# Kernel optimization log

Measured on AMD Instinct MI355X. Metric: run time of the kernel, lower is better.

## Reference

```python
import jax, jax.numpy as jnp
import numpy as np

N_HEAD = 16
QK_NOPE = 128
QK_ROPE = 64
QK_HEAD = QK_NOPE + QK_ROPE  # 192
V_HEAD = 128
SCALE = 1.0 / np.sqrt(QK_HEAD)


def setup_inputs() -> dict:
    key = jax.random.key(0)
    ks = jax.random.split(key, 8)
    B, T, C = 2, 2048, 2048
    s = lambda fan: 1.0 / np.sqrt(fan)
    return {
        "x": jax.random.normal(ks[0], (B, T, C), jnp.float32),
        "freqs_cis": jax.random.uniform(ks[1], (T, QK_ROPE // 2, 2), jnp.float32),
        "w_q": jax.random.normal(ks[2], (C, N_HEAD * QK_HEAD), jnp.float32) * s(C),
        "w_kv_down": jax.random.normal(ks[3], (C, 256), jnp.float32) * s(C),
        "w_k_up": jax.random.normal(ks[4], (256, N_HEAD * QK_HEAD), jnp.float32) * s(256),
        "w_v_up": jax.random.normal(ks[5], (256, N_HEAD * V_HEAD), jnp.float32) * s(256),
        "w_o": jax.random.normal(ks[6], (N_HEAD * V_HEAD, C), jnp.float32) * s(N_HEAD * V_HEAD),
        "start_pos": 0,
    }


def _rotate_half(x):
    x1, x2 = x[..., : x.shape[-1] // 2], x[..., x.shape[-1] // 2 :]
    return jnp.concatenate([-x2, x1], axis=-1)


def reference(x, freqs_cis, w_q, w_kv_down, w_k_up, w_v_up, w_o, start_pos):
    B, T, C = x.shape
    # low-rank MLA projections
    q = (x @ w_q).reshape(B, T, N_HEAD, QK_HEAD)
    kv = x @ w_kv_down                                  # (B,T,r)
    k = (kv @ w_k_up).reshape(B, T, N_HEAD, QK_HEAD)
    v = (kv @ w_v_up).reshape(B, T, N_HEAD, V_HEAD)

    # inline RoPE on decoupled rope dims
    q_nope, q_rope = q[..., :QK_NOPE], q[..., QK_NOPE:]
    k_nope, k_rope = k[..., :QK_NOPE], k[..., QK_NOPE:]
    freqs = freqs_cis[start_pos : start_pos + T]         # (T, 32, 2)
    cos = freqs[..., 0][None, :, None, :]                # (1,T,1,32)
    sin = freqs[..., 1][None, :, None, :]
    rep = QK_ROPE // cos.shape[-1]
    cos = jnp.tile(cos, (1, 1, 1, rep))                  # (1,T,1,64)
    sin = jnp.tile(sin, (1, 1, 1, rep))
    q_rope = q_rope * cos + _rotate_half(q_rope) * sin
    k_rope = k_rope * cos + _rotate_half(k_rope) * sin
    q = jnp.concatenate([q_nope, q_rope], axis=-1)
    k = jnp.concatenate([k_nope, k_rope], axis=-1)

    # causal SDPA with mismatched QK vs V head dims
    scores = jnp.einsum("bqhd,bkhd->bhqk", q, k) * SCALE
    causal = jnp.tril(jnp.ones((T, T), dtype=bool))
    scores = jnp.where(causal[None, None], scores, -jnp.inf)
    probs = jax.nn.softmax(scores, axis=-1)
    out = jnp.einsum("bhqk,bkhd->bqhd", probs, v)        # (B,T,H,V_HEAD)
    out = out.reshape(B, T, N_HEAD * V_HEAD)
    return out @ w_o
```

## Files before the change

### kernel.cpp

```cpp
#include <hip/hip_runtime.h>
#include <stdint.h>

typedef unsigned short u16;
typedef float f32x4 __attribute__((ext_vector_type(4)));
typedef __bf16 bf16x8 __attribute__((ext_vector_type(8)));

static __device__ __forceinline__ u16 f2bf(float f) {
  union { float f; unsigned u; } v; v.f = f;
  unsigned r = v.u + 0x7fffu + ((v.u >> 16) & 1u);
  return (u16)(r >> 16);
}
static __device__ __forceinline__ float bf2f(u16 h) {
  union { unsigned u; float f; } v; v.u = ((unsigned)h) << 16;
  return v.f;
}

#define GLD_LDS16(gp, lp) __builtin_amdgcn_global_load_lds( \
    (__attribute__((address_space(1))) void*)(gp),          \
    (__attribute__((address_space(3))) void*)(lp), 16, 0, 0)

#define MFMA16(a, b, c) __builtin_amdgcn_mfma_f32_16x16x32_bf16((a), (b), (c), 0, 0, 0)

__global__ void conv_bf16_kernel(const float* __restrict__ in, u16* __restrict__ out, long n) {
  long stride = (long)gridDim.x * blockDim.x * 4;
  for (long i = ((long)blockIdx.x * blockDim.x + threadIdx.x) * 4; i < n; i += stride) {
    float4 v = *(const float4*)(in + i);
    union { u16 s[4]; uint2 u; } pk;
    pk.s[0] = f2bf(v.x); pk.s[1] = f2bf(v.y); pk.s[2] = f2bf(v.z); pk.s[3] = f2bf(v.w);
    *(uint2*)(out + i) = pk.u;
  }
}

__global__ void transpose_conv_kernel(const float* __restrict__ W, u16* __restrict__ WT,
                                      int K, int N) {
  __shared__ float tile[32][33];
  const int n0 = blockIdx.x * 32, k0 = blockIdx.y * 32;
  const int tx = threadIdx.x, ty = threadIdx.y;
#pragma unroll
  for (int i = 0; i < 32; i += 8) tile[ty + i][tx] = W[(long)(k0 + ty + i) * N + n0 + tx];
  __syncthreads();
#pragma unroll
  for (int i = 0; i < 32; i += 8)
    WT[(long)(n0 + ty + i) * K + k0 + tx] = f2bf(tile[tx][ty + i]);
}

template <bool OUT_F32>
__global__ __launch_bounds__(256, 2)
void gemm_bt_kernel(const u16* __restrict__ A, const u16* __restrict__ BT,
                    void* __restrict__ Cv, int N, int K, long sA, long sB, long sC) {
  const int bz = blockIdx.z;
  A += (long)bz * sA;
  BT += (long)bz * sB;
  const int m0 = blockIdx.y << 7, n0 = blockIdx.x << 7;
  __shared__ alignas(16) u16 lA[128 * 64];
  __shared__ alignas(16) u16 lB[128 * 64];
  const int tid = threadIdx.x;
  const int w = tid >> 6, l = tid & 63;
  const int wr = w >> 1, wc = w & 1;
  const int lrow = l & 15, lg = l >> 4;
  const int srow = l >> 3, scol = (l & 7) << 3;
  f32x4 acc[4][4] = {};
  for (int kt = 0; kt < K; kt += 64) {
    __syncthreads();
#pragma unroll
    for (int i = 0; i < 4; i++) {
      const int chunk = (w << 2) + i;
      const int row = (chunk << 3) + srow;
      GLD_LDS16(A + (long)(m0 + row) * K + kt + scol, &lA[chunk << 9]);
      GLD_LDS16(BT + (long)(n0 + row) * K + kt + scol, &lB[chunk << 9]);
    }
    __syncthreads();
#pragma unroll
    for (int kk = 0; kk < 2; kk++) {
      bf16x8 af[4], bb[4];
#pragma unroll
      for (int i = 0; i < 4; i++) {
        af[i] = *(const bf16x8*)&lA[((wr << 6) + (i << 4) + lrow) * 64 + (kk << 5) + (lg << 3)];
        bb[i] = *(const bf16x8*)&lB[((wc << 6) + (i << 4) + lrow) * 64 + (kk << 5) + (lg << 3)];
      }
#pragma unroll
      for (int mi = 0; mi < 4; mi++)
#pragma unroll
        for (int ni = 0; ni < 4; ni++)
          acc[mi][ni] = MFMA16(af[mi], bb[ni], acc[mi][ni]);
    }
  }
#pragma unroll
  for (int mi = 0; mi < 4; mi++) {
    const int r0 = m0 + (wr << 6) + (mi << 4) + (lg << 2);
#pragma unroll
    for (int ni = 0; ni < 4; ni++) {
      const int c0 = n0 + (wc << 6) + (ni << 4) + lrow;
#pragma unroll
      for (int r = 0; r < 4; r++) {
        const float val = acc[mi][ni][r];
        if constexpr (OUT_F32)
          ((float*)Cv + (long)bz * sC)[(long)(r0 + r) * N + c0] = val;
        else
          ((u16*)Cv + (long)bz * sC)[(long)(r0 + r) * N + c0] = f2bf(val);
      }
    }
  }
}

__device__ __forceinline__ void epilogue_rope_store(
    u16* __restrict__ C, const int N, const f32x4 (*acc)[4],
    const int m0, const int wr, const int wc, const int cbase_wave,
    const int lrow, const int lg, const bool ropewin,
    const float* __restrict__ freqs, const int sp) {
#pragma unroll
  for (int mi = 0; mi < 4; mi++) {
    const int r0 = m0 + (wr << 6) + (mi << 4) + (lg << 2);
#pragma unroll
    for (int r = 0; r < 4; r++) {
      float v0 = acc[mi][0][r], v1 = acc[mi][1][r];
      float v2 = acc[mi][2][r], v3 = acc[mi][3][r];
      if (ropewin) {
        const int t = (r0 + r) & 2047;
        const float2 cs0 = *(const float2*)&freqs[((long)(sp + t) * 32 + lrow) * 2];
        const float2 cs1 = *(const float2*)&freqs[((long)(sp + t) * 32 + 16 + lrow) * 2];
        const float n0v = v0 * cs0.x - v2 * cs0.y;
        const float n1v = v1 * cs1.x - v3 * cs1.y;
        const float n2v = v2 * cs0.x + v0 * cs0.y;
        const float n3v = v3 * cs1.x + v1 * cs1.y;
        v0 = n0v; v1 = n1v; v2 = n2v; v3 = n3v;
      }
      const long ro = (long)(r0 + r) * N + cbase_wave + lrow;
      C[ro] = f2bf(v0);
      C[ro + 16] = f2bf(v1);
      C[ro + 32] = f2bf(v2);
      C[ro + 48] = f2bf(v3);
    }
  }
}

__global__ __launch_bounds__(256, 2)
void gemm_q_kvd_kernel(const u16* __restrict__ A, const u16* __restrict__ wqT,
                       const u16* __restrict__ wkdT, u16* __restrict__ qb,
                       u16* __restrict__ kvb,
                       const float* __restrict__ freqs, const int* __restrict__ sp_ptr) {
  constexpr int K = 2048;
  const int m0 = blockIdx.y << 7;
  const int n0raw = blockIdx.x << 7;
  const bool is_kv = n0raw >= 3072;
  const u16* BT = is_kv ? (wkdT + (long)(n0raw - 3072) * K) : (wqT + (long)n0raw * K);
  u16* C = is_kv ? kvb : qb;
  const int N = is_kv ? 256 : 3072;
  const int c_base = is_kv ? (n0raw - 3072) : n0raw;
  __shared__ alignas(16) u16 lA[128 * 64];
  __shared__ alignas(16) u16 lB[128 * 64];
  const int tid = threadIdx.x;
  const int w = tid >> 6, l = tid & 63;
  const int wr = w >> 1, wc = w & 1;
  const int lrow = l & 15, lg = l >> 4;
  const int srow = l >> 3, scol = (l & 7) << 3;
  f32x4 acc[4][4] = {};
  for (int kt = 0; kt < K; kt += 64) {
    __syncthreads();
#pragma unroll
    for (int i = 0; i < 4; i++) {
      const int chunk = (w << 2) + i;
      const int row = (chunk << 3) + srow;
      GLD_LDS16(A + (long)(m0 + row) * K + kt + scol, &lA[chunk << 9]);
      GLD_LDS16(BT + (long)row * K + kt + scol, &lB[chunk << 9]);
    }
    __syncthreads();
#pragma unroll
    for (int kk = 0; kk < 2; kk++) {
      bf16x8 af[4], bb[4];
#pragma unroll
      for (int i = 0; i < 4; i++) {
        af[i] = *(const bf16x8*)&lA[((wr << 6) + (i << 4) + lrow) * 64 + (kk << 5) + (lg << 3)];
        bb[i] = *(const bf16x8*)&lB[((wc << 6) + (i << 4) + lrow) * 64 + (kk << 5) + (lg << 3)];
      }
#pragma unroll
      for (int mi = 0; mi < 4; mi++)
#pragma unroll
        for (int ni = 0; ni < 4; ni++)
          acc[mi][ni] = MFMA16(af[mi], bb[ni], acc[mi][ni]);
    }
  }
  const int cbase_wave = c_base + (wc << 6);
  const bool ropewin = (!is_kv) && (cbase_wave % 192 == 128);
  const int sp = sp_ptr[0];
  epilogue_rope_store(C, N, acc, m0, wr, wc, cbase_wave, lrow, lg, ropewin, freqs, sp);
}

__global__ __launch_bounds__(256, 2)
void gemm_kup_vt_kernel(const u16* __restrict__ kvb, const u16* __restrict__ wkuT,
                        const u16* __restrict__ wvuT, u16* __restrict__ kb,
                        u16* __restrict__ vTb,
                        const float* __restrict__ freqs, const int* __restrict__ sp_ptr) {
  constexpr int K = 256;
  const int bid = blockIdx.x;
  const u16 *A, *BT;
  u16* C;
  int N, m0, n0;
  bool is_k;
  if (bid < 768) {
    A = kvb; BT = wkuT; C = kb; N = 3072;
    m0 = (bid / 24) << 7; n0 = (bid % 24) << 7;
    is_k = true;
  } else {
    int r = bid - 768;
    const int bz = r >> 8;
    r &= 255;
    A = wvuT; BT = kvb + (long)bz * 2048 * 256; C = vTb + (long)bz * 2048 * 2048;
    N = 2048;
    m0 = (r >> 4) << 7; n0 = (r & 15) << 7;
    is_k = false;
  }
  __shared__ alignas(16) u16 lA[128 * 64];
  __shared__ alignas(16) u16 lB[128 * 64];
  const int tid = threadIdx.x;
  const int w = tid >> 6, l = tid & 63;
  const int wr = w >> 1, wc = w & 1;
  const int lrow = l & 15, lg = l >> 4;
  const int srow = l >> 3, scol = (l & 7) << 3;
  f32x4 acc[4][4] = {};
  for (int kt = 0; kt < K; kt += 64) {
    __syncthreads();
#pragma unroll
    for (int i = 0; i < 4; i++) {
      const int chunk = (w << 2) + i;
      const int row = (chunk << 3) + srow;
      GLD_LDS16(A + (long)(m0 + row) * K + kt + scol, &lA[chunk << 9]);
      GLD_LDS16(BT + (long)(n0 + row) * K + kt + scol, &lB[chunk << 9]);
    }
    __syncthreads();
#pragma unroll
    for (int kk = 0; kk < 2; kk++) {
      bf16x8 af[4], bb[4];
#pragma unroll
      for (int i = 0; i < 4; i++) {
        af[i] = *(const bf16x8*)&lA[((wr << 6) + (i << 4) + lrow) * 64 + (kk << 5) + (lg << 3)];
        bb[i] = *(const bf16x8*)&lB[((wc << 6) + (i << 4) + lrow) * 64 + (kk << 5) + (lg << 3)];
      }
#pragma unroll
      for (int mi = 0; mi < 4; mi++)
#pragma unroll
        for (int ni = 0; ni < 4; ni++)
          acc[mi][ni] = MFMA16(af[mi], bb[ni], acc[mi][ni]);
    }
  }
  const int cbase_wave = n0 + (wc << 6);
  const bool ropewin = is_k && (cbase_wave % 192 == 128);
  const int sp = sp_ptr[0];
  epilogue_rope_store(C, N, acc, m0, wr, wc, cbase_wave, lrow, lg, ropewin, freqs, sp);
}


__device__ __forceinline__ void attn_tile_step(
    const bf16x8* __restrict__ qf, f32x4* __restrict__ o, float* __restrict__ l_part,
    const int qrb, const int t0,
    const u16* __restrict__ Kl, const u16* __restrict__ Vl,
    u16* __restrict__ pw, const int lrow, const int lg) {
  constexpr float SCALE = 0.07216878364870323f;
  f32x4 s[4];
  __builtin_amdgcn_s_setprio(1);
#pragma unroll
  for (int tb = 0; tb < 4; tb++) {
    f32x4 a = {};
#pragma unroll
    for (int kb = 0; kb < 6; kb++) {
      bf16x8 kf = *(const bf16x8*)&Kl[((tb << 4) + lrow) * 200 + (kb << 5) + (lg << 3)];
      a = MFMA16(qf[kb], kf, a);
    }
    s[tb] = a;
  }
  __builtin_amdgcn_s_setprio(0);
#pragma unroll
  for (int tb = 0; tb < 4; tb++) {
    const int tt = t0 + (tb << 4) + lrow;
#pragma unroll
    for (int r = 0; r < 4; r++) {
      const int qrow = qrb + (lg << 2) + r;
      float p = __expf(s[tb][r] * SCALE);
      p = (tt <= qrow) ? p : 0.f;
      s[tb][r] = p;
      l_part[r] += p;
    }
  }
#pragma unroll
  for (int tb = 0; tb < 4; tb++)
#pragma unroll
    for (int r = 0; r < 4; r++)
      pw[((lg << 2) + r) * 68 + (tb << 4) + lrow] = f2bf(s[tb][r]);
  bf16x8 pf0 = *(const bf16x8*)&pw[lrow * 68 + (lg << 3)];
  bf16x8 pf1 = *(const bf16x8*)&pw[lrow * 68 + 32 + (lg << 3)];
  __builtin_amdgcn_s_setprio(1);
#pragma unroll
  for (int db = 0; db < 8; db++) {
    bf16x8 v0 = *(const bf16x8*)&Vl[((db << 4) + lrow) * 72 + (lg << 3)];
    bf16x8 v1 = *(const bf16x8*)&Vl[((db << 4) + lrow) * 72 + 32 + (lg << 3)];
    o[db] = MFMA16(pf0, v0, o[db]);
    o[db] = MFMA16(pf1, v1, o[db]);
  }
  __builtin_amdgcn_s_setprio(0);
}

__device__ __forceinline__ void attn_tile_step2(
    const bf16x8* __restrict__ qfA, const bf16x8* __restrict__ qfB,
    f32x4* __restrict__ oA, f32x4* __restrict__ oB,
    float* __restrict__ lpA, float* __restrict__ lpB,
    const int qrbA, const int qrbB, const int t0,
    const u16* __restrict__ Kl, const u16* __restrict__ Vl,
    u16* __restrict__ pwA, u16* __restrict__ pwB, const int lrow, const int lg) {
  constexpr float SCALE = 0.07216878364870323f;
  f32x4 sA[4], sB[4];
  __builtin_amdgcn_s_setprio(1);
#pragma unroll
  for (int tb = 0; tb < 4; tb++) {
    f32x4 a = {}, bq = {};
#pragma unroll
    for (int kb = 0; kb < 6; kb++) {
      bf16x8 kf = *(const bf16x8*)&Kl[((tb << 4) + lrow) * 200 + (kb << 5) + (lg << 3)];
      a = MFMA16(qfA[kb], kf, a);
      bq = MFMA16(qfB[kb], kf, bq);
    }
    sA[tb] = a;
    sB[tb] = bq;
  }
  __builtin_amdgcn_s_setprio(0);
#pragma unroll
  for (int tb = 0; tb < 4; tb++) {
    const int tt = t0 + (tb << 4) + lrow;
#pragma unroll
    for (int r = 0; r < 4; r++) {
      const int qrowA = qrbA + (lg << 2) + r;
      float pA = __expf(sA[tb][r] * SCALE);
      pA = (tt <= qrowA) ? pA : 0.f;
      sA[tb][r] = pA;
      lpA[r] += pA;
      const int qrowB = qrbB + (lg << 2) + r;
      float pB = __expf(sB[tb][r] * SCALE);
      pB = (tt <= qrowB) ? pB : 0.f;
      sB[tb][r] = pB;
      lpB[r] += pB;
    }
  }
#pragma unroll
  for (int tb = 0; tb < 4; tb++)
#pragma unroll
    for (int r = 0; r < 4; r++) {
      pwA[((lg << 2) + r) * 68 + (tb << 4) + lrow] = f2bf(sA[tb][r]);
      pwB[((lg << 2) + r) * 68 + (tb << 4) + lrow] = f2bf(sB[tb][r]);
    }
  bf16x8 pfA0 = *(const bf16x8*)&pwA[lrow * 68 + (lg << 3)];
  bf16x8 pfA1 = *(const bf16x8*)&pwA[lrow * 68 + 32 + (lg << 3)];
  bf16x8 pfB0 = *(const bf16x8*)&pwB[lrow * 68 + (lg << 3)];
  bf16x8 pfB1 = *(const bf16x8*)&pwB[lrow * 68 + 32 + (lg << 3)];
  __builtin_amdgcn_s_setprio(1);
#pragma unroll
  for (int db = 0; db < 8; db++) {
    bf16x8 v0 = *(const bf16x8*)&Vl[((db << 4) + lrow) * 72 + (lg << 3)];
    bf16x8 v1 = *(const bf16x8*)&Vl[((db << 4) + lrow) * 72 + 32 + (lg << 3)];
    oA[db] = MFMA16(pfA0, v0, oA[db]);
    oB[db] = MFMA16(pfB0, v0, oB[db]);
    oA[db] = MFMA16(pfA1, v1, oA[db]);
    oB[db] = MFMA16(pfB1, v1, oB[db]);
  }
  __builtin_amdgcn_s_setprio(0);
}

__device__ __forceinline__ void attn_write(
    u16* __restrict__ ob, const f32x4* __restrict__ o, const float* __restrict__ l_part,
    const int lrow, const int lg) {
#pragma unroll
  for (int r = 0; r < 4; r++) {
    float l = l_part[r];
#pragma unroll
    for (int d = 1; d < 16; d <<= 1) l += __shfl_xor(l, d);
    const float inv = 1.f / l;
#pragma unroll
    for (int db = 0; db < 8; db++)
      ob[(long)((lg << 2) + r) * 2048 + (db << 4) + lrow] = f2bf(o[db][r] * inv);
  }
}

__global__ __launch_bounds__(256, 2)
void attn_kernel(const u16* __restrict__ q, const u16* __restrict__ k,
                 const u16* __restrict__ vT, u16* __restrict__ out) {
  const int bid = blockIdx.x;
  const int xcd = bid & 7;
  const int rest = bid >> 3;
  const int pair = rest & 15;
  const int bh = ((rest >> 4) << 3) | xcd;
  const int b = bh >> 4, h = bh & 15;
  const int tid = threadIdx.x, w = tid >> 6, l = tid & 63;
  const int lrow = l & 15, lg = l >> 4;
  const int qtA = pair, qtB = 31 - pair;
  const int qrbA = (qtA << 6) + (w << 4);
  const int qrbB = (qtB << 6) + (w << 4);
  __shared__ alignas(16) u16 Kl[64 * 200];
  __shared__ alignas(16) u16 Vl[128 * 72];
  __shared__ alignas(16) u16 Pl[4][2][16 * 68];

  bf16x8 qfA[6], qfB[6];
  {
    const u16* qbA = q + ((long)b * 2048 + qrbA + lrow) * 3072 + h * 192;
    const u16* qbB = q + ((long)b * 2048 + qrbB + lrow) * 3072 + h * 192;
#pragma unroll
    for (int kb = 0; kb < 6; kb++) {
      qfA[kb] = *(const bf16x8*)&qbA[(kb << 5) + (lg << 3)];
      qfB[kb] = *(const bf16x8*)&qbB[(kb << 5) + (lg << 3)];
    }
  }
  f32x4 oA[8] = {}, oB[8] = {};
  float lA[4] = {}, lB[4] = {};

  const u16* kbh = k + (long)b * 2048 * 3072 + h * 192;
  const u16* vbh = vT + ((long)b * 2048 + h * 128) * 2048;
  const int tEndA = qtA << 6, tEndB = qtB << 6;

  for (int t0 = 0; t0 <= tEndB; t0 += 64) {
    __syncthreads();
#pragma unroll
    for (int i = 0; i < 6; i++) {
      int c = (i << 8) + tid;
      int row = c / 24, col = (c % 24) << 3;
      *(bf16x8*)&Kl[row * 200 + col] = *(const bf16x8*)&kbh[(long)(t0 + row) * 3072 + col];
    }
#pragma unroll
    for (int i = 0; i < 4; i++) {
      int c = (i << 8) + tid;
      int row = c >> 3, col = (c & 7) << 3;
      *(bf16x8*)&Vl[row * 72 + col] = *(const bf16x8*)&vbh[(long)row * 2048 + t0 + col];
    }
    __syncthreads();
    if (t0 <= tEndA)
      attn_tile_step2(qfA, qfB, oA, oB, lA, lB, qrbA, qrbB, t0, Kl, Vl,
                      &Pl[w][0][0], &Pl[w][1][0], lrow, lg);
    else
      attn_tile_step(qfB, oB, lB, qrbB, t0, Kl, Vl, &Pl[w][1][0], lrow, lg);
  }
  attn_write(out + ((long)b * 2048 + qrbA) * 2048 + (h << 7), oA, lA, lrow, lg);
  attn_write(out + ((long)b * 2048 + qrbB) * 2048 + (h << 7), oB, lB, lrow, lg);
}

extern "C" void kernel_launch(void* const* d_in, const int* in_sizes, int n_in,
                              void* d_out, int out_size, void* d_ws, size_t ws_size,
                              hipStream_t stream) {
  const float* x = (const float*)d_in[0];
  const float* fcis = (const float*)d_in[1];
  const float* w_q = (const float*)d_in[2];
  const float* w_kvd = (const float*)d_in[3];
  const float* w_ku = (const float*)d_in[4];
  const float* w_vu = (const float*)d_in[5];
  const float* w_o = (const float*)d_in[6];
  const int* start_pos = (const int*)d_in[7];
  float* out = (float*)d_out;

  char* p = (char*)d_ws;
  auto alloc = [&](long bytes) -> char* {
    char* r = p;
    p += (bytes + 255) & ~255ll;
    return r;
  };
  u16* xb = (u16*)alloc(4096ll * 2048 * 2);
  u16* wqT = (u16*)alloc(3072ll * 2048 * 2);
  u16* wkdT = (u16*)alloc(256ll * 2048 * 2);
  u16* wkuT = (u16*)alloc(3072ll * 256 * 2);
  u16* wvuT = (u16*)alloc(2048ll * 256 * 2);
  u16* woT = (u16*)alloc(2048ll * 2048 * 2);
  u16* qb = (u16*)alloc(4096ll * 3072 * 2);
  u16* kvb = (u16*)alloc(4096ll * 256 * 2);
  u16* kb = (u16*)alloc(4096ll * 3072 * 2);
  u16* aob = (u16*)alloc(4096ll * 2048 * 2);
  u16* vTb = xb;

  conv_bf16_kernel<<<2048, 256, 0, stream>>>(x, xb, 4096ll * 2048);
  dim3 tb(32, 8);
  transpose_conv_kernel<<<dim3(3072 / 32, 2048 / 32), tb, 0, stream>>>(w_q, wqT, 2048, 3072);
  transpose_conv_kernel<<<dim3(256 / 32, 2048 / 32), tb, 0, stream>>>(w_kvd, wkdT, 2048, 256);
  transpose_conv_kernel<<<dim3(3072 / 32, 256 / 32), tb, 0, stream>>>(w_ku, wkuT, 256, 3072);
  transpose_conv_kernel<<<dim3(2048 / 32, 256 / 32), tb, 0, stream>>>(w_vu, wvuT, 256, 2048);
  transpose_conv_kernel<<<dim3(2048 / 32, 2048 / 32), tb, 0, stream>>>(w_o, woT, 2048, 2048);

  gemm_q_kvd_kernel<<<dim3(26, 32), 256, 0, stream>>>(xb, wqT, wkdT, qb, kvb, fcis, start_pos);
  gemm_kup_vt_kernel<<<1280, 256, 0, stream>>>(kvb, wkuT, wvuT, kb, vTb, fcis, start_pos);
  attn_kernel<<<512, 256, 0, stream>>>(qb, kb, vTb, aob);
  gemm_bt_kernel<true><<<dim3(16, 32, 1), 256, 0, stream>>>(aob, woT, out, 2048, 2048, 0, 0, 0);
}
```

Baseline: 288.1 us.

## Fuse prep conversions into one launch and remap GEMM tiles per XCD

Merges the x-to-bf16 conversion and the five weight transpose-conversions into a single prep kernel, which removes five kernel launches. It also remaps the block indices of the three GEMM kernels so that each XCD (blocks taken as bid mod 8) gets a contiguous group of M tiles, aiming to improve reuse in the per-XCD L2 cache. The output GEMM becomes a dedicated non-templated kernel with a 1D grid that uses the same swizzle. The change relies on the 1D grid count matching the tile counts exactly.

```diff
diff --git a/kernel.cpp b/kernel.cpp
--- a/kernel.cpp
+++ b/kernel.cpp
@@ -21,86 +21,41 @@
 
 #define MFMA16(a, b, c) __builtin_amdgcn_mfma_f32_16x16x32_bf16((a), (b), (c), 0, 0, 0)
 
-__global__ void conv_bf16_kernel(const float* __restrict__ in, u16* __restrict__ out, long n) {
-  long stride = (long)gridDim.x * blockDim.x * 4;
-  for (long i = ((long)blockIdx.x * blockDim.x + threadIdx.x) * 4; i < n; i += stride) {
-    float4 v = *(const float4*)(in + i);
-    union { u16 s[4]; uint2 u; } pk;
-    pk.s[0] = f2bf(v.x); pk.s[1] = f2bf(v.y); pk.s[2] = f2bf(v.z); pk.s[3] = f2bf(v.w);
-    *(uint2*)(out + i) = pk.u;
-  }
-}
-
-__global__ void transpose_conv_kernel(const float* __restrict__ W, u16* __restrict__ WT,
-                                      int K, int N) {
+__global__ void prep_kernel(const float* __restrict__ x, u16* __restrict__ xb,
+                            const float* __restrict__ w_q, u16* __restrict__ wqT,
+                            const float* __restrict__ w_kvd, u16* __restrict__ wkdT,
+                            const float* __restrict__ w_ku, u16* __restrict__ wkuT,
+                            const float* __restrict__ w_vu, u16* __restrict__ wvuT,
+                            const float* __restrict__ w_o, u16* __restrict__ woT) {
   __shared__ float tile[32][33];
-  const int n0 = blockIdx.x * 32, k0 = blockIdx.y * 32;
+  const int bid = blockIdx.x;
   const int tx = threadIdx.x, ty = threadIdx.y;
+  if (bid < 2048) {
+    const int tid = ty * 32 + tx;
+    const long n = 4096ll * 2048;
+    const long stride = 2048ll * 256 * 4;
+    for (long i = ((long)bid * 256 + tid) * 4; i < n; i += stride) {
+      float4 v = *(const float4*)(x + i);
+      union { u16 s[4]; uint2 u; } pk;
+      pk.s[0] = f2bf(v.x); pk.s[1] = f2bf(v.y); pk.s[2] = f2bf(v.z); pk.s[3] = f2bf(v.w);
+      *(uint2*)(xb + i) = pk.u;
+    }
+    return;
+  }
+  const float* W; u16* WT; int K, N, bx, by;
+  int r = bid - 2048;
+  if (r < 6144)        { W = w_q;   WT = wqT;  K = 2048; N = 3072; bx = r % 96; by = r / 96; }
+  else if ((r -= 6144) < 512) { W = w_kvd; WT = wkdT; K = 2048; N = 256;  bx = r % 8;  by = r / 8; }
+  else if ((r -= 512) < 768)  { W = w_ku;  WT = wkuT; K = 256;  N = 3072; bx = r % 96; by = r / 96; }
+  else if ((r -= 768) < 512)  { W = w_vu;  WT = wvuT; K = 256;  N = 2048; bx = r % 64; by = r / 64; }
+  else                 { r -= 512; W = w_o; WT = woT; K = 2048; N = 2048; bx = r % 64; by = r / 64; }
+  const int n0 = bx * 32, k0 = by * 32;
 #pragma unroll
   for (int i = 0; i < 32; i += 8) tile[ty + i][tx] = W[(long)(k0 + ty + i) * N + n0 + tx];
   __syncthreads();
 #pragma unroll
   for (int i = 0; i < 32; i += 8)
     WT[(long)(n0 + ty + i) * K + k0 + tx] = f2bf(tile[tx][ty + i]);
-}
-
-template <bool OUT_F32>
-__global__ __launch_bounds__(256, 2)
-void gemm_bt_kernel(const u16* __restrict__ A, const u16* __restrict__ BT,
-                    void* __restrict__ Cv, int N, int K, long sA, long sB, long sC) {
-  const int bz = blockIdx.z;
-  A += (long)bz * sA;
-  BT += (long)bz * sB;
-  const int m0 = blockIdx.y << 7, n0 = blockIdx.x << 7;
-  __shared__ alignas(16) u16 lA[128 * 64];
-  __shared__ alignas(16) u16 lB[128 * 64];
-  const int tid = threadIdx.x;
-  const int w = tid >> 6, l = tid & 63;
-  const int wr = w >> 1, wc = w & 1;
-  const int lrow = l & 15, lg = l >> 4;
-  const int srow = l >> 3, scol = (l & 7) << 3;
-  f32x4 acc[4][4] = {};
-  for (int kt = 0; kt < K; kt += 64) {
-    __syncthreads();
-#pragma unroll
-    for (int i = 0; i < 4; i++) {
-      const int chunk = (w << 2) + i;
-      const int row = (chunk << 3) + srow;
-      GLD_LDS16(A + (long)(m0 + row) * K + kt + scol, &lA[chunk << 9]);
-      GLD_LDS16(BT + (long)(n0 + row) * K + kt + scol, &lB[chunk << 9]);
-    }
-    __syncthreads();
-#pragma unroll
-    for (int kk = 0; kk < 2; kk++) {
-      bf16x8 af[4], bb[4];
-#pragma unroll
-      for (int i = 0; i < 4; i++) {
-        af[i] = *(const bf16x8*)&lA[((wr << 6) + (i << 4) + lrow) * 64 + (kk << 5) + (lg << 3)];
-        bb[i] = *(const bf16x8*)&lB[((wc << 6) + (i << 4) + lrow) * 64 + (kk << 5) + (lg << 3)];
-      }
-#pragma unroll
-      for (int mi = 0; mi < 4; mi++)
-#pragma unroll
-        for (int ni = 0; ni < 4; ni++)
-          acc[mi][ni] = MFMA16(af[mi], bb[ni], acc[mi][ni]);
-    }
-  }
-#pragma unroll
-  for (int mi = 0; mi < 4; mi++) {
-    const int r0 = m0 + (wr << 6) + (mi << 4) + (lg << 2);
-#pragma unroll
-    for (int ni = 0; ni < 4; ni++) {
-      const int c0 = n0 + (wc << 6) + (ni << 4) + lrow;
-#pragma unroll
-      for (int r = 0; r < 4; r++) {
-        const float val = acc[mi][ni][r];
-        if constexpr (OUT_F32)
-          ((float*)Cv + (long)bz * sC)[(long)(r0 + r) * N + c0] = val;
-        else
-          ((u16*)Cv + (long)bz * sC)[(long)(r0 + r) * N + c0] = f2bf(val);
-      }
-    }
-  }
 }
 
 __device__ __forceinline__ void epilogue_rope_store(
@@ -140,8 +95,11 @@
                        u16* __restrict__ kvb,
                        const float* __restrict__ freqs, const int* __restrict__ sp_ptr) {
   constexpr int K = 2048;
-  const int m0 = blockIdx.y << 7;
-  const int n0raw = blockIdx.x << 7;
+  const int bid = blockIdx.x;
+  const int xcd = bid & 7;
+  const int idx = bid >> 3;
+  const int m0 = ((xcd << 2) + (idx & 3)) << 7;
+  const int n0raw = (idx >> 2) << 7;
   const bool is_kv = n0raw >= 3072;
   const u16* BT = is_kv ? (wkdT + (long)(n0raw - 3072) * K) : (wqT + (long)n0raw * K);
   u16* C = is_kv ? kvb : qb;
@@ -198,16 +156,20 @@
   int N, m0, n0;
   bool is_k;
   if (bid < 768) {
+    const int xcd = bid & 7, idx = bid >> 3;
     A = kvb; BT = wkuT; C = kb; N = 3072;
-    m0 = (bid / 24) << 7; n0 = (bid % 24) << 7;
+    m0 = ((xcd << 2) + (idx & 3)) << 7;
+    n0 = (idx >> 2) << 7;
     is_k = true;
   } else {
-    int r = bid - 768;
-    const int bz = r >> 8;
-    r &= 255;
+    const int r = bid - 768;
+    const int xcd = r & 7, idx = r >> 3;
+    const int mt = (xcd << 1) + (idx & 1);
+    const int rest = idx >> 1;
+    const int nt = rest & 15, bz = rest >> 4;
     A = wvuT; BT = kvb + (long)bz * 2048 * 256; C = vTb + (long)bz * 2048 * 2048;
     N = 2048;
-    m0 = (r >> 4) << 7; n0 = (r & 15) << 7;
+    m0 = mt << 7; n0 = nt << 7;
     is_k = false;
   }
   __shared__ alignas(16) u16 lA[128 * 64];
@@ -247,6 +209,60 @@
   const bool ropewin = is_k && (cbase_wave % 192 == 128);
   const int sp = sp_ptr[0];
   epilogue_rope_store(C, N, acc, m0, wr, wc, cbase_wave, lrow, lg, ropewin, freqs, sp);
+}
+
+__global__ __launch_bounds__(256, 2)
+void gemm_out_kernel(const u16* __restrict__ A, const u16* __restrict__ BT,
+                     float* __restrict__ C) {
+  constexpr int K = 2048, N = 2048;
+  const int bid = blockIdx.x;
+  const int xcd = bid & 7, idx = bid >> 3;
+  const int m0 = ((xcd << 2) + (idx & 3)) << 7;
+  const int n0 = (idx >> 2) << 7;
+  __shared__ alignas(16) u16 lA[128 * 64];
+  __shared__ alignas(16) u16 lB[128 * 64];
+  const int tid = threadIdx.x;
+  const int w = tid >> 6, l = tid & 63;
+  const int wr = w >> 1, wc = w & 1;
+  const int lrow = l & 15, lg = l >> 4;
+  const int srow = l >> 3, scol = (l & 7) << 3;
+  f32x4 acc[4][4] = {};
+  for (int kt = 0; kt < K; kt += 64) {
+    __syncthreads();
+#pragma unroll
+    for (int i = 0; i < 4; i++) {
+      const int chunk = (w << 2) + i;
+      const int row = (chunk << 3) + srow;
+      GLD_LDS16(A + (long)(m0 + row) * K + kt + scol, &lA[chunk << 9]);
+      GLD_LDS16(BT + (long)(n0 + row) * K + kt + scol, &lB[chunk << 9]);
+    }
+    __syncthreads();
+#pragma unroll
+    for (int kk = 0; kk < 2; kk++) {
+      bf16x8 af[4], bb[4];
+#pragma unroll
+      for (int i = 0; i < 4; i++) {
+        af[i] = *(const bf16x8*)&lA[((wr << 6) + (i << 4) + lrow) * 64 + (kk << 5) + (lg << 3)];
+        bb[i] = *(const bf16x8*)&lB[((wc << 6) + (i << 4) + lrow) * 64 + (kk << 5) + (lg << 3)];
+      }
+#pragma unroll
+      for (int mi = 0; mi < 4; mi++)
+#pragma unroll
+        for (int ni = 0; ni < 4; ni++)
+          acc[mi][ni] = MFMA16(af[mi], bb[ni], acc[mi][ni]);
+    }
+  }
+#pragma unroll
+  for (int mi = 0; mi < 4; mi++) {
+    const int r0 = m0 + (wr << 6) + (mi << 4) + (lg << 2);
+#pragma unroll
+    for (int ni = 0; ni < 4; ni++) {
+      const int c0 = n0 + (wc << 6) + (ni << 4) + lrow;
+#pragma unroll
+      for (int r = 0; r < 4; r++)
+        C[(long)(r0 + r) * N + c0] = acc[mi][ni][r];
+    }
+  }
 }
 
 
@@ -469,16 +485,10 @@
   u16* aob = (u16*)alloc(4096ll * 2048 * 2);
   u16* vTb = xb;
 
-  conv_bf16_kernel<<<2048, 256, 0, stream>>>(x, xb, 4096ll * 2048);
-  dim3 tb(32, 8);
-  transpose_conv_kernel<<<dim3(3072 / 32, 2048 / 32), tb, 0, stream>>>(w_q, wqT, 2048, 3072);
-  transpose_conv_kernel<<<dim3(256 / 32, 2048 / 32), tb, 0, stream>>>(w_kvd, wkdT, 2048, 256);
-  transpose_conv_kernel<<<dim3(3072 / 32, 256 / 32), tb, 0, stream>>>(w_ku, wkuT, 256, 3072);
-  transpose_conv_kernel<<<dim3(2048 / 32, 256 / 32), tb, 0, stream>>>(w_vu, wvuT, 256, 2048);
-  transpose_conv_kernel<<<dim3(2048 / 32, 2048 / 32), tb, 0, stream>>>(w_o, woT, 2048, 2048);
-
-  gemm_q_kvd_kernel<<<dim3(26, 32), 256, 0, stream>>>(xb, wqT, wkdT, qb, kvb, fcis, start_pos);
+  prep_kernel<<<14080, dim3(32, 8), 0, stream>>>(x, xb, w_q, wqT, w_kvd, wkdT,
+                                                 w_ku, wkuT, w_vu, wvuT, w_o, woT);
+  gemm_q_kvd_kernel<<<832, 256, 0, stream>>>(xb, wqT, wkdT, qb, kvb, fcis, start_pos);
   gemm_kup_vt_kernel<<<1280, 256, 0, stream>>>(kvb, wkuT, wvuT, kb, vTb, fcis, start_pos);
   attn_kernel<<<512, 256, 0, stream>>>(qb, kb, vTb, aob);
-  gemm_bt_kernel<true><<<dim3(16, 32, 1), 256, 0, stream>>>(aob, woT, out, 2048, 2048, 0, 0, 0);
-}
+  gemm_out_kernel<<<512, 256, 0, stream>>>(aob, woT, out);
+}
```

After: 274.1 us. 4.9% less time.
